# Kernel tuning notes

Measured on AMD Instinct MI355X. Metric: run time of the kernel, lower is better.

## Reference

```python
import jax, jax.numpy as jnp
import numpy as np

B, N, E, F, D = 8, 2000, 64000, 1024, 128
NEG_SLOPE = 0.01  # torch LeakyReLU default

def leaky(x):
    return jnp.where(x >= 0, x, NEG_SLOPE * x)

def gcn_conv(x, ei, W, b):
    # PyG GCNConv: add self loops, symmetric norm, x @ W, scatter-sum, + bias
    src, tgt = ei[0], ei[1]
    loops = jnp.arange(N, dtype=src.dtype)
    src_a = jnp.concatenate([src, loops])
    tgt_a = jnp.concatenate([tgt, loops])
    deg = jax.ops.segment_sum(jnp.ones(src_a.shape, x.dtype), tgt_a, num_segments=N)
    dinv = jnp.where(deg > 0, jax.lax.rsqrt(deg), 0.0)
    norm = dinv[src_a] * dinv[tgt_a]  # [E+N]
    h = x @ W                          # [N, F]
    out = jax.ops.segment_sum(norm[:, None] * h[src_a], tgt_a, num_segments=N)
    return out + b

gcn_conv_b = jax.vmap(gcn_conv, in_axes=(0, 0, None, None))

def setup_inputs() -> dict:
    key = jax.random.key(0)
    ks = jax.random.split(key, 16)
    s = lambda fan: 1.0 / np.sqrt(fan)
    return {
        "x1": jax.random.normal(ks[0], (B, N, F), jnp.float32),
        "ei1": jax.random.randint(ks[1], (B, 2, E), 0, N, jnp.int32),
        "x2": jax.random.normal(ks[2], (B, N, F), jnp.float32),
        "ei2": jax.random.randint(ks[3], (B, 2, E), 0, N, jnp.int32),
        "Wg1": jax.random.normal(ks[4], (F, F), jnp.float32) * s(F),
        "bg1": jnp.zeros((F,), jnp.float32),
        "Wf1": jax.random.normal(ks[5], (F, D), jnp.float32) * s(F),
        "bf1": jnp.zeros((D,), jnp.float32),
        "Wg2": jax.random.normal(ks[6], (F, F), jnp.float32) * s(F),
        "bg2": jnp.zeros((F,), jnp.float32),
        "Wf2": jax.random.normal(ks[7], (F, D), jnp.float32) * s(F),
        "bf2": jnp.zeros((D,), jnp.float32),
        "W1": jax.random.normal(ks[8], (2 * D, 256), jnp.float32) * s(2 * D),
        "b1": jnp.zeros((256,), jnp.float32),
        "W2": jax.random.normal(ks[9], (256, 64), jnp.float32) * s(256),
        "b2": jnp.zeros((64,), jnp.float32),
        "Wo": jax.random.normal(ks[10], (64, 1), jnp.float32) * s(64),
        "bo": jnp.zeros((1,), jnp.float32),
    }

def reference(x1, ei1, x2, ei2, Wg1, bg1, Wf1, bf1, Wg2, bg2, Wf2, bf2,
              W1, b1, W2, b2, Wo, bo):
    # branch 1
    h1 = leaky(gcn_conv_b(x1, ei1, Wg1, bg1))       # [B, N, F]
    g1 = jnp.mean(h1, axis=1)                        # [B, F]
    g1 = leaky(g1 @ Wf1 + bf1)                       # [B, D] (dropout = eval identity)
    # branch 2
    h2 = leaky(gcn_conv_b(x2, ei2, Wg2, bg2))
    g2 = jnp.mean(h2, axis=1)
    g2 = leaky(g2 @ Wf2 + bf2)
    # head
    xc = jnp.concatenate([g1, g2], axis=1)           # [B, 2D]
    xc = leaky(xc @ W1 + b1)
    xc = leaky(xc @ W2 + b2)
    return jax.nn.sigmoid(xc @ Wo + bo)              # [B, 1]
```

## Files before the change

### kernel.cpp

```cpp
#include <hip/hip_runtime.h>
#include <stdint.h>

#define B 8
#define NN 2000
#define EG 64000
#define FF 1024
#define DD 128
#define BK 32
#define NCHUNK 125
#define CG 5

#define NB_CONV 32000
#define NB_WT   2048
#define NB_DEG  4000
#define NTK 16
#define NB_G8 504

typedef short short8 __attribute__((ext_vector_type(8)));
typedef float f32x4 __attribute__((ext_vector_type(4)));
typedef float f32x2 __attribute__((ext_vector_type(2)));

__device__ __forceinline__ unsigned short f2bf(float f) {
    union { float f; unsigned int u; } v; v.f = f;
    unsigned int u = v.u;
    unsigned int r = u + 0x7FFFu + ((u >> 16) & 1u);
    return (unsigned short)(r >> 16);
}
__device__ __forceinline__ float leaky(float v) { return v >= 0.0f ? v : 0.01f * v; }

__device__ __forceinline__ void acc8p(f32x2* __restrict__ r, float w, uint4 v) {
    union { unsigned int u; float f; } c;
    f32x2 wv = {w, w};
    f32x2 h;
    c.u = v.x << 16;          h.x = c.f;
    c.u = v.x & 0xffff0000u;  h.y = c.f;
    r[0] += wv * h;
    c.u = v.y << 16;          h.x = c.f;
    c.u = v.y & 0xffff0000u;  h.y = c.f;
    r[1] += wv * h;
    c.u = v.z << 16;          h.x = c.f;
    c.u = v.z & 0xffff0000u;  h.y = c.f;
    r[2] += wv * h;
    c.u = v.w << 16;          h.x = c.f;
    c.u = v.w & 0xffff0000u;  h.y = c.f;
    r[3] += wv * h;
}

__global__ void k_prep(const float* __restrict__ x_a, const float* __restrict__ x_b,
                       unsigned short* __restrict__ xb,
                       const float* __restrict__ Wg_a, const float* __restrict__ Wg_b,
                       unsigned short* __restrict__ wT,
                       const int* __restrict__ ei_a, const int* __restrict__ ei_b,
                       int* __restrict__ degi) {
    int blk = blockIdx.x;
    int tid = threadIdx.x;
    __shared__ float tile[32][33];
    if (blk < NB_CONV) {
        int i = blk * 256 + tid;
        float4 v = (i < NB_CONV * 128) ? ((const float4*)x_a)[i]
                                       : ((const float4*)x_b)[i - NB_CONV * 128];
        ushort4 o;
        o.x = f2bf(v.x); o.y = f2bf(v.y); o.z = f2bf(v.z); o.w = f2bf(v.w);
        ((ushort4*)xb)[i] = o;
    } else if (blk < NB_CONV + NB_WT) {
        int b2 = blk - NB_CONV;
        int z = b2 >> 10, rem = b2 & 1023;
        int by = rem >> 5, bx = rem & 31;
        int tx = tid & 31, ty = tid >> 5;
        int k0 = by * 32, n0 = bx * 32;
        const float* Wg = z ? Wg_b : Wg_a;
        unsigned short* o = wT + (size_t)z * FF * FF;
#pragma unroll
        for (int r = 0; r < 4; ++r) {
            int row = ty + r * 8;
            tile[row][tx] = Wg[(k0 + row) * FF + n0 + tx];
        }
        __syncthreads();
#pragma unroll
        for (int r = 0; r < 4; ++r) {
            int row = ty + r * 8;
            o[(n0 + row) * FF + k0 + tx] = f2bf(tile[tx][row]);
        }
    } else {
        int i = (blk - NB_CONV - NB_WT) * 256 + tid;
        int g = i / EG, e = i - g * EG;
        const int* ei = (g < B) ? (ei_a + (size_t)g * 2 * EG)
                                : (ei_b + (size_t)(g - B) * 2 * EG);
        int t = ei[EG + e];
        atomicAdd(&degi[g * NN + t], 1);
    }
}

__global__ void k_scan(const int* __restrict__ degi, int* __restrict__ csr_off,
                       int* __restrict__ cursor, float* __restrict__ dinv) {
    int g = blockIdx.x, t = threadIdx.x;
    __shared__ int part[256];
    int loc[8];
    int s = 0;
#pragma unroll
    for (int i = 0; i < 8; ++i) {
        int n = t * 8 + i;
        int c = (n < NN) ? degi[g * NN + n] : 0;
        if (n < NN) dinv[g * NN + n] = rsqrtf((float)(c + 1));
        loc[i] = s;
        s += c;
    }
    part[t] = s;
    __syncthreads();
    for (int off = 1; off < 256; off <<= 1) {
        int v = (t >= off) ? part[t - off] : 0;
        __syncthreads();
        part[t] += v;
        __syncthreads();
    }
    int base = part[t] - s;
#pragma unroll
    for (int i = 0; i < 8; ++i) {
        int n = t * 8 + i;
        if (n < NN) {
            int o = base + loc[i];
            csr_off[g * (NN + 1) + n] = o;
            cursor[g * NN + n] = o;
        }
    }
    if (t == 255) csr_off[g * (NN + 1) + NN] = part[255];
}

__launch_bounds__(512, 2) __global__
void k_gemm8(const unsigned short* __restrict__ Abf, const unsigned short* __restrict__ wT,
             unsigned short* __restrict__ Hbf,
             const int* __restrict__ ei_a, const int* __restrict__ ei_b,
             int* __restrict__ cursor, const float* __restrict__ dinv,
             int2* __restrict__ epk) {
    __shared__ __align__(16) char smem[131072];
    int bid = blockIdx.x;
    int wg = (bid & 7) * 63 + (bid >> 3);
    int mt = wg >> 2, nt = wg & 3;
    int set = (mt >= 63) ? 1 : 0;
    int m0 = set * 16000 + (mt - set * 63) * 256;
    int n0 = nt * 256;
    int mlim = set * 16000 + 16000;
    const unsigned short* Bg = wT + (size_t)set * FF * FF;

    int tid = threadIdx.x;
    int lane = tid & 63, wave = tid >> 6;
    int wr = wave >> 2, wc = wave & 3;
    int l15 = lane & 15, q = lane >> 4;
    int qx = q ^ (((l15 >> 2) & 1) << 1);
    int arow = wr * 128 + l15;
    int brow = wc * 64 + l15;
    int col8s = (tid & 7) ^ (((tid >> 5) & 1) << 1);
    int srow = tid >> 3;
    unsigned wbase = (unsigned)wave << 10;

    f32x4 acc[8][4];
#pragma unroll
    for (int i = 0; i < 8; ++i)
#pragma unroll
        for (int j = 0; j < 4; ++j) acc[i][j] = (f32x4){0.f, 0.f, 0.f, 0.f};

    auto stage = [&](int ktn, int isB, int hh) {
        const unsigned short* gsrc = isB ? Bg : Abf;
        int x0 = isB ? n0 : m0;
        int r1 = x0 + hh * 128 + srow;
        int kb = ktn * 64 + col8s * 8;
        unsigned db = ((unsigned)(ktn & 1) << 16) | ((unsigned)isB << 15)
                    | ((unsigned)hh << 14) | wbase;
        __builtin_amdgcn_global_load_lds(
            (const __attribute__((address_space(1))) unsigned int*)(gsrc + (size_t)r1 * FF + kb),
            (__attribute__((address_space(3))) unsigned int*)&smem[db], 16, 0, 0);
        __builtin_amdgcn_global_load_lds(
            (const __attribute__((address_space(1))) unsigned int*)(gsrc + (size_t)(r1 + 64) * FF + kb),
            (__attribute__((address_space(3))) unsigned int*)&smem[db + 8192], 16, 0, 0);
    };

    stage(0, 0, 0); stage(0, 0, 1); stage(0, 1, 0); stage(0, 1, 1);

    unsigned bb = 0;
    auto lda = [&](int i, int kk) -> short8 {
        return *(const short8*)&smem[bb + ((unsigned)(arow + i * 16) << 7)
                                        + ((unsigned)(kk * 4 + qx) << 4)];
    };
    auto ldb = [&](int j, int kk) -> short8 {
        return *(const short8*)&smem[bb + 32768u + ((unsigned)(brow + j * 16) << 7)
                                        + ((unsigned)(kk * 4 + qx) << 4)];
    };

    for (int kt = 0; kt < NTK; ++kt) {
        asm volatile("s_waitcnt vmcnt(0)" ::: "memory");
        __builtin_amdgcn_s_barrier();
        bb = (unsigned)(kt & 1) << 16;
        short8 fa[4], fb[4];
#pragma unroll
        for (int j = 0; j < 4; ++j) fb[j] = ldb(j, 0);
#pragma unroll
        for (int i = 0; i < 4; ++i) fa[i] = lda(i, 0);
        if (kt + 1 < NTK) stage(kt + 1, 0, 0);
        __builtin_amdgcn_s_barrier();
        asm volatile("s_waitcnt lgkmcnt(0)" ::: "memory");
        __builtin_amdgcn_sched_barrier(0);
        __builtin_amdgcn_s_setprio(1);
#pragma unroll
        for (int i = 0; i < 4; ++i)
#pragma unroll
            for (int j = 0; j < 4; ++j)
                acc[i][j] = __builtin_amdgcn_mfma_f32_16x16x32_bf16(fa[i], fb[j], acc[i][j], 0, 0, 0);
        __builtin_amdgcn_s_setprio(0);
        __builtin_amdgcn_s_barrier();
#pragma unroll
        for (int i = 0; i < 4; ++i) fa[i] = lda(i + 4, 0);
        if (kt + 1 < NTK) stage(kt + 1, 0, 1);
        __builtin_amdgcn_s_barrier();
        asm volatile("s_waitcnt lgkmcnt(0)" ::: "memory");
        __builtin_amdgcn_sched_barrier(0);
        __builtin_amdgcn_s_setprio(1);
#pragma unroll
        for (int i = 0; i < 4; ++i)
#pragma unroll
            for (int j = 0; j < 4; ++j)
                acc[i + 4][j] = __builtin_amdgcn_mfma_f32_16x16x32_bf16(fa[i], fb[j], acc[i + 4][j], 0, 0, 0);
        __builtin_amdgcn_s_setprio(0);
        __builtin_amdgcn_s_barrier();
#pragma unroll
        for (int j = 0; j < 4; ++j) fb[j] = ldb(j, 1);
#pragma unroll
        for (int i = 0; i < 4; ++i) fa[i] = lda(i, 1);
        if (kt + 1 < NTK) stage(kt + 1, 1, 0);
        __builtin_amdgcn_s_barrier();
        asm volatile("s_waitcnt lgkmcnt(0)" ::: "memory");
        __builtin_amdgcn_sched_barrier(0);
        __builtin_amdgcn_s_setprio(1);
#pragma unroll
        for (int i = 0; i < 4; ++i)
#pragma unroll
            for (int j = 0; j < 4; ++j)
                acc[i][j] = __builtin_amdgcn_mfma_f32_16x16x32_bf16(fa[i], fb[j], acc[i][j], 0, 0, 0);
        __builtin_amdgcn_s_setprio(0);
        __builtin_amdgcn_s_barrier();
#pragma unroll
        for (int i = 0; i < 4; ++i) fa[i] = lda(i + 4, 1);
        if (kt + 1 < NTK) stage(kt + 1, 1, 1);
        __builtin_amdgcn_s_barrier();
        asm volatile("s_waitcnt lgkmcnt(0)" ::: "memory");
        __builtin_amdgcn_sched_barrier(0);
        __builtin_amdgcn_s_setprio(1);
#pragma unroll
        for (int i = 0; i < 4; ++i)
#pragma unroll
            for (int j = 0; j < 4; ++j)
                acc[i + 4][j] = __builtin_amdgcn_mfma_f32_16x16x32_bf16(fa[i], fb[j], acc[i + 4][j], 0, 0, 0);
        __builtin_amdgcn_s_setprio(0);
        __builtin_amdgcn_s_barrier();
    }

#pragma unroll
    for (int i = 0; i < 8; ++i) {
#pragma unroll
        for (int j = 0; j < 4; ++j) {
            int n = n0 + wc * 64 + j * 16 + l15;
#pragma unroll
            for (int v = 0; v < 4; ++v) {
                int m = m0 + wr * 128 + i * 16 + q * 4 + v;
                if (m < mlim) Hbf[(size_t)m * FF + n] = f2bf(acc[i][j][v]);
            }
        }
    }

    int ebase = bid * 512 + tid;
#pragma unroll
    for (int r = 0; r < 4; ++r) {
        int idx = ebase + r * (NB_G8 * 512);
        if (idx < 16 * EG) {
            int gg = idx / EG, e = idx - gg * EG;
            const int* ei = (gg < B) ? (ei_a + (size_t)gg * 2 * EG)
                                     : (ei_b + (size_t)(gg - B) * 2 * EG);
            int s = ei[e];
            int t = ei[EG + e];
            int pos = atomicAdd(&cursor[gg * NN + t], 1);
            int2 p;
            p.x = s;
            p.y = __float_as_int(dinv[gg * NN + s] * dinv[gg * NN + t]);
            epk[(size_t)gg * EG + pos] = p;
        }
    }
}

__launch_bounds__(256) __global__
void k_aggreduce(const unsigned short* __restrict__ Hbf, const int* __restrict__ csr_off,
                 const int2* __restrict__ epk, const float* __restrict__ dinv,
                 const float* __restrict__ bg_a, const float* __restrict__ bg_b,
                 float* __restrict__ part) {
    int blk = blockIdx.x;
    int phase = blk / 1000;
    int bp = blk - phase * 1000;
    int half = phase & 1;
    int g = (phase >> 1) * 8 + (bp & 7);
    int chunk = bp >> 3;
    int tid = threadIdx.x;
    int team = tid >> 6;
    int lane = tid & 63;
    int f0 = half * 512 + lane * 8;
    int n0 = chunk * 16 + team * 4;
    const unsigned short* Hb = Hbf + (size_t)g * NN * FF;
    const int2* ep = epk + (size_t)g * EG;
    const float* bg = (g < B) ? bg_a : bg_b;

    f32x2 bgv[4];
#pragma unroll
    for (int i = 0; i < 4; ++i) bgv[i] = (f32x2){bg[f0 + 2 * i], bg[f0 + 2 * i + 1]};
    f32x2 bsum[4];
#pragma unroll
    for (int i = 0; i < 4; ++i) bsum[i] = (f32x2){0.f, 0.f};

    for (int nn = 0; nn < 4; ++nn) {
        int n = n0 + nn;
        float dn = dinv[g * NN + n];
        int beg = csr_off[g * (NN + 1) + n];
        int end = csr_off[g * (NN + 1) + n + 1];
        f32x2 racc[4];
#pragma unroll
        for (int i = 0; i < 4; ++i) racc[i] = (f32x2){0.f, 0.f};
        {
            uint4 sv = *(const uint4*)&Hb[(n << 10) + f0];
            acc8p(racc, dn * dn, sv);
        }
        int j = beg;
        int2 pe0, pe1, pe2, pe3;
        if (j + 4 <= end) { pe0 = ep[j]; pe1 = ep[j + 1]; pe2 = ep[j + 2]; pe3 = ep[j + 3]; }
        for (; j + 8 <= end; j += 4) {
            int2 e0 = pe0, e1 = pe1, e2 = pe2, e3 = pe3;
            pe0 = ep[j + 4]; pe1 = ep[j + 5]; pe2 = ep[j + 6]; pe3 = ep[j + 7];
            uint4 v0 = *(const uint4*)&Hb[(e0.x << 10) + f0];
            uint4 v1 = *(const uint4*)&Hb[(e1.x << 10) + f0];
            uint4 v2 = *(const uint4*)&Hb[(e2.x << 10) + f0];
            uint4 v3 = *(const uint4*)&Hb[(e3.x << 10) + f0];
            acc8p(racc, __int_as_float(e0.y), v0);
            acc8p(racc, __int_as_float(e1.y), v1);
            acc8p(racc, __int_as_float(e2.y), v2);
            acc8p(racc, __int_as_float(e3.y), v3);
        }
        if (j + 4 <= end) {
            uint4 v0 = *(const uint4*)&Hb[(pe0.x << 10) + f0];
            uint4 v1 = *(const uint4*)&Hb[(pe1.x << 10) + f0];
            uint4 v2 = *(const uint4*)&Hb[(pe2.x << 10) + f0];
            uint4 v3 = *(const uint4*)&Hb[(pe3.x << 10) + f0];
            acc8p(racc, __int_as_float(pe0.y), v0);
            acc8p(racc, __int_as_float(pe1.y), v1);
            acc8p(racc, __int_as_float(pe2.y), v2);
            acc8p(racc, __int_as_float(pe3.y), v3);
            j += 4;
        }
        for (; j < end; ++j) {
            int2 e = ep[j];
            uint4 v = *(const uint4*)&Hb[(e.x << 10) + f0];
            acc8p(racc, __int_as_float(e.y), v);
        }
#pragma unroll
        for (int i = 0; i < 4; ++i) {
            f32x2 t = racc[i] + bgv[i];
            bsum[i].x += leaky(t.x);
            bsum[i].y += leaky(t.y);
        }
    }

    __shared__ float red[3][64 * 9];
    if (team > 0) {
#pragma unroll
        for (int i = 0; i < 4; ++i) {
            red[team - 1][lane * 9 + 2 * i]     = bsum[i].x;
            red[team - 1][lane * 9 + 2 * i + 1] = bsum[i].y;
        }
    }
    __syncthreads();
    if (team == 0) {
        float* o = part + ((size_t)g * NCHUNK + chunk) * FF + f0;
        float r[8];
#pragma unroll
        for (int i = 0; i < 4; ++i) {
            r[2 * i]     = bsum[i].x;
            r[2 * i + 1] = bsum[i].y;
        }
#pragma unroll
        for (int t = 0; t < 3; ++t)
#pragma unroll
            for (int i = 0; i < 8; ++i) r[i] += red[t][lane * 9 + i];
        float4 a = {r[0], r[1], r[2], r[3]};
        float4 c = {r[4], r[5], r[6], r[7]};
        *(float4*)&o[0] = a;
        *(float4*)&o[4] = c;
    }
}

__global__ void k_gsum1(const float* __restrict__ part, float* __restrict__ part2) {
    int blk = blockIdx.x;
    int g = blk / 20;
    int rem = blk - g * 20;
    int fq = rem / CG, cg = rem - fq * CG;
    int f = fq * 256 + threadIdx.x;
    const float* p = part + (size_t)g * NCHUNK * FF + (size_t)cg * 25 * FF + f;
    float s = 0.f;
#pragma unroll 5
    for (int c = 0; c < 25; ++c) s += p[(size_t)c * FF];
    part2[((size_t)g * CG + cg) * FF + f] = s;
}

__launch_bounds__(512) __global__
void k_fc(const float* __restrict__ part2, const float* __restrict__ Wf_a,
          const float* __restrict__ bf_a, const float* __restrict__ Wf_b,
          const float* __restrict__ bf_b, float* __restrict__ g12) {
    int g = blockIdx.x, t = threadIdx.x;
    int d = t & 127, slice = t >> 7;
    __shared__ float gs[FF];
    __shared__ float red[4][DD];
    const float* p = part2 + (size_t)g * CG * FF;
#pragma unroll
    for (int i = 0; i < 2; ++i) {
        int f = i * 512 + t;
        float s = 0.f;
#pragma unroll
        for (int c = 0; c < CG; ++c) s += p[(size_t)c * FF + f];
        gs[f] = s;
    }
    __syncthreads();
    const float* Wf = (g < B) ? Wf_a : Wf_b;
    const float* bfv = (g < B) ? bf_a : bf_b;
    float acc = 0.f;
    int fbase = slice * 256;
#pragma unroll 8
    for (int ff = 0; ff < 256; ++ff) {
        int f = fbase + ff;
        acc += gs[f] * Wf[f * DD + d];
    }
    red[slice][d] = acc;
    __syncthreads();
    if (t < DD) {
        float a = red[0][t] + red[1][t] + red[2][t] + red[3][t];
        a = a * (1.0f / (float)NN) + bfv[t];
        g12[g * DD + t] = leaky(a);
    }
}

__launch_bounds__(256) __global__
void k_head(const float* __restrict__ g, const float* __restrict__ W1, const float* __restrict__ b1,
            const float* __restrict__ W2, const float* __restrict__ b2,
            const float* __restrict__ Wo, const float* __restrict__ bo, float* __restrict__ out) {
    __shared__ float xc[8][256];
    __shared__ float l1[8][256];
    __shared__ float l2[8][64];
    int t = threadIdx.x;
#pragma unroll
    for (int i = 0; i < 8; ++i) {
        int idx = i * 256 + t;
        int b = idx >> 8, j = idx & 255;
        xc[b][j] = (j < DD) ? g[b * DD + j] : g[B * DD + b * DD + (j - DD)];
    }
    __syncthreads();
    {
        int j = t;
        float a[8];
#pragma unroll
        for (int b = 0; b < 8; ++b) a[b] = b1[j];
        for (int k = 0; k < 256; ++k) {
            float w = W1[k * 256 + j];
#pragma unroll
            for (int b = 0; b < 8; ++b) a[b] += xc[b][k] * w;
        }
#pragma unroll
        for (int b = 0; b < 8; ++b) l1[b][j] = leaky(a[b]);
    }
    __syncthreads();
    if (t < 64) {
        int j = t;
        float a[8];
#pragma unroll
        for (int b = 0; b < 8; ++b) a[b] = b2[j];
        for (int k = 0; k < 256; ++k) {
            float w = W2[k * 64 + j];
#pragma unroll
            for (int b = 0; b < 8; ++b) a[b] += l1[b][k] * w;
        }
#pragma unroll
        for (int b = 0; b < 8; ++b) l2[b][j] = leaky(a[b]);
    }
    __syncthreads();
    if (t < 8) {
        float a = bo[0];
        for (int k = 0; k < 64; ++k) a += l2[t][k] * Wo[k];
        out[t] = 1.0f / (1.0f + expf(-a));
    }
}

extern "C" void kernel_launch(void* const* d_in, const int* in_sizes, int n_in,
                              void* d_out, int out_size, void* d_ws, size_t ws_size,
                              hipStream_t stream) {
    const float* x1  = (const float*)d_in[0];
    const int*   ei1 = (const int*)d_in[1];
    const float* x2  = (const float*)d_in[2];
    const int*   ei2 = (const int*)d_in[3];
    const float* Wg1 = (const float*)d_in[4];
    const float* bg1 = (const float*)d_in[5];
    const float* Wf1 = (const float*)d_in[6];
    const float* bf1 = (const float*)d_in[7];
    const float* Wg2 = (const float*)d_in[8];
    const float* bg2 = (const float*)d_in[9];
    const float* Wf2 = (const float*)d_in[10];
    const float* bf2 = (const float*)d_in[11];
    const float* W1  = (const float*)d_in[12];
    const float* b1  = (const float*)d_in[13];
    const float* W2  = (const float*)d_in[14];
    const float* b2  = (const float*)d_in[15];
    const float* Wo  = (const float*)d_in[16];
    const float* bo  = (const float*)d_in[17];
    float* out = (float*)d_out;

    auto align = [](size_t v) { return (v + 255) & ~(size_t)255; };
    size_t need = 0;
    size_t o_deg  = need; need += align((size_t)16 * NN * 4);
    size_t o_dinv = need; need += align((size_t)16 * NN * 4);
    size_t o_csr  = need; need += align((size_t)16 * (NN + 1) * 4);
    size_t o_cur  = need; need += align((size_t)16 * NN * 4);
    size_t o_epk  = need; need += align((size_t)16 * EG * 8);
    size_t o_xbf  = need; need += align(((size_t)16 * NN + 128) * FF * 2);
    size_t o_wT   = need; need += align((size_t)2 * FF * FF * 2);
    size_t o_hbf  = need; need += align((size_t)16 * NN * FF * 2);
    size_t o_part = need; need += align((size_t)16 * NCHUNK * FF * 4);
    size_t o_pt2  = need; need += align((size_t)16 * CG * FF * 4);
    size_t o_g12  = need; need += align((size_t)16 * DD * 4);
    (void)need;

    char* w = (char*)d_ws;
    int* degi    = (int*)(w + o_deg);
    float* dinv  = (float*)(w + o_dinv);
    int* csr     = (int*)(w + o_csr);
    int* cur     = (int*)(w + o_cur);
    int2* epk    = (int2*)(w + o_epk);
    unsigned short* xbf = (unsigned short*)(w + o_xbf);
    unsigned short* wT  = (unsigned short*)(w + o_wT);
    unsigned short* hbf = (unsigned short*)(w + o_hbf);
    float* part  = (float*)(w + o_part);
    float* part2 = (float*)(w + o_pt2);
    float* g12   = (float*)(w + o_g12);

    hipMemsetAsync(degi, 0, (size_t)16 * NN * 4, stream);
    k_prep<<<NB_CONV + NB_WT + NB_DEG, 256, 0, stream>>>(x1, x2, xbf, Wg1, Wg2, wT,
                                                         ei1, ei2, degi);
    k_scan<<<16, 256, 0, stream>>>(degi, csr, cur, dinv);
    k_gemm8<<<NB_G8, 512, 0, stream>>>(xbf, wT, hbf, ei1, ei2, cur, dinv, epk);
    k_aggreduce<<<4000, 256, 0, stream>>>(hbf, csr, epk, dinv, bg1, bg2, part);
    k_gsum1<<<16 * 20, 256, 0, stream>>>(part, part2);
    k_fc<<<16, 512, 0, stream>>>(part2, Wf1, bf1, Wf2, bf2, g12);
    k_head<<<1, 256, 0, stream>>>(g12, W1, b1, W2, b2, Wo, bo, out);
}
```

Before: 544.0 us.

## Rework GEMM LDS swizzle, stage ordering and partial vmcnt waits

Changes the LDS XOR swizzle to an 8-way row-based pattern and precomputes the swizzled column offsets for each k-half. The staging order now loads B before A, and rows are split so each stage covers interleaved 64-row halves. The full vmcnt(0) wait at the top of each k-iteration is replaced by partial vmcnt(2) waits placed mid-iteration, so compute can begin once only part of the tile has landed. This is meant to reduce LDS bank conflicts and shorten stalls on global-to-LDS loads, but it makes the wait accounting fragile.

```diff
diff --git a/kernel.cpp b/kernel.cpp
--- a/kernel.cpp
+++ b/kernel.cpp
@@ -6,7 +6,6 @@
 #define EG 64000
 #define FF 1024
 #define DD 128
-#define BK 32
 #define NCHUNK 125
 #define CG 5
 
@@ -146,11 +145,13 @@
     int lane = tid & 63, wave = tid >> 6;
     int wr = wave >> 2, wc = wave & 3;
     int l15 = lane & 15, q = lane >> 4;
-    int qx = q ^ (((l15 >> 2) & 1) << 1);
     int arow = wr * 128 + l15;
     int brow = wc * 64 + l15;
-    int col8s = (tid & 7) ^ (((tid >> 5) & 1) << 1);
+    int sw = l15 & 7;
+    unsigned so0 = (unsigned)((q ^ sw) << 4);
+    unsigned so1 = (unsigned)(((4 + q) ^ sw) << 4);
     int srow = tid >> 3;
+    int col8s = (tid & 7) ^ (srow & 7);
     unsigned wbase = (unsigned)wave << 10;
 
     f32x4 acc[8][4];
@@ -159,43 +160,44 @@
 #pragma unroll
         for (int j = 0; j < 4; ++j) acc[i][j] = (f32x4){0.f, 0.f, 0.f, 0.f};
 
-    auto stage = [&](int ktn, int isB, int hh) {
+    auto stage = [&](int ktn, int isB, int h) {
         const unsigned short* gsrc = isB ? Bg : Abf;
         int x0 = isB ? n0 : m0;
-        int r1 = x0 + hh * 128 + srow;
+        int r1 = x0 + h * 64 + srow;
         int kb = ktn * 64 + col8s * 8;
         unsigned db = ((unsigned)(ktn & 1) << 16) | ((unsigned)isB << 15)
-                    | ((unsigned)hh << 14) | wbase;
+                    | ((unsigned)h << 13) | wbase | ((unsigned)(tid & 7) << 4)
+                    ;
+        db = ((unsigned)(ktn & 1) << 16) | ((unsigned)isB << 15)
+           | ((unsigned)h << 13) | wbase;
         __builtin_amdgcn_global_load_lds(
             (const __attribute__((address_space(1))) unsigned int*)(gsrc + (size_t)r1 * FF + kb),
             (__attribute__((address_space(3))) unsigned int*)&smem[db], 16, 0, 0);
         __builtin_amdgcn_global_load_lds(
-            (const __attribute__((address_space(1))) unsigned int*)(gsrc + (size_t)(r1 + 64) * FF + kb),
-            (__attribute__((address_space(3))) unsigned int*)&smem[db + 8192], 16, 0, 0);
+            (const __attribute__((address_space(1))) unsigned int*)(gsrc + (size_t)(r1 + 128) * FF + kb),
+            (__attribute__((address_space(3))) unsigned int*)&smem[db + 16384], 16, 0, 0);
     };
 
-    stage(0, 0, 0); stage(0, 0, 1); stage(0, 1, 0); stage(0, 1, 1);
+    stage(0, 1, 0); stage(0, 1, 1); stage(0, 0, 0); stage(0, 0, 1);
+    asm volatile("s_waitcnt vmcnt(2)" ::: "memory");
+    __builtin_amdgcn_s_barrier();
 
     unsigned bb = 0;
-    auto lda = [&](int i, int kk) -> short8 {
-        return *(const short8*)&smem[bb + ((unsigned)(arow + i * 16) << 7)
-                                        + ((unsigned)(kk * 4 + qx) << 4)];
+    auto lda = [&](int i, unsigned so) -> short8 {
+        return *(const short8*)&smem[bb + ((unsigned)(arow + i * 16) << 7) + so];
     };
-    auto ldb = [&](int j, int kk) -> short8 {
-        return *(const short8*)&smem[bb + 32768u + ((unsigned)(brow + j * 16) << 7)
-                                        + ((unsigned)(kk * 4 + qx) << 4)];
+    auto ldb = [&](int j, unsigned so) -> short8 {
+        return *(const short8*)&smem[bb + 32768u + ((unsigned)(brow + j * 16) << 7) + so];
     };
 
     for (int kt = 0; kt < NTK; ++kt) {
-        asm volatile("s_waitcnt vmcnt(0)" ::: "memory");
-        __builtin_amdgcn_s_barrier();
         bb = (unsigned)(kt & 1) << 16;
         short8 fa[4], fb[4];
 #pragma unroll
-        for (int j = 0; j < 4; ++j) fb[j] = ldb(j, 0);
-#pragma unroll
-        for (int i = 0; i < 4; ++i) fa[i] = lda(i, 0);
-        if (kt + 1 < NTK) stage(kt + 1, 0, 0);
+        for (int j = 0; j < 4; ++j) fb[j] = ldb(j, so0);
+#pragma unroll
+        for (int i = 0; i < 4; ++i) fa[i] = lda(i, so0);
+        if (kt + 1 < NTK) stage(kt + 1, 1, 0);
         __builtin_amdgcn_s_barrier();
         asm volatile("s_waitcnt lgkmcnt(0)" ::: "memory");
         __builtin_amdgcn_sched_barrier(0);
@@ -206,10 +208,12 @@
             for (int j = 0; j < 4; ++j)
                 acc[i][j] = __builtin_amdgcn_mfma_f32_16x16x32_bf16(fa[i], fb[j], acc[i][j], 0, 0, 0);
         __builtin_amdgcn_s_setprio(0);
-        __builtin_amdgcn_s_barrier();
-#pragma unroll
-        for (int i = 0; i < 4; ++i) fa[i] = lda(i + 4, 0);
-        if (kt + 1 < NTK) stage(kt + 1, 0, 1);
+        if (kt + 1 < NTK) asm volatile("s_waitcnt vmcnt(2)" ::: "memory");
+        else              asm volatile("s_waitcnt vmcnt(0)" ::: "memory");
+        __builtin_amdgcn_s_barrier();
+#pragma unroll
+        for (int i = 0; i < 4; ++i) fa[i] = lda(i + 4, so0);
+        if (kt + 1 < NTK) stage(kt + 1, 1, 1);
         __builtin_amdgcn_s_barrier();
         asm volatile("s_waitcnt lgkmcnt(0)" ::: "memory");
         __builtin_amdgcn_sched_barrier(0);
@@ -222,10 +226,10 @@
         __builtin_amdgcn_s_setprio(0);
         __builtin_amdgcn_s_barrier();
 #pragma unroll
-        for (int j = 0; j < 4; ++j) fb[j] = ldb(j, 1);
-#pragma unroll
-        for (int i = 0; i < 4; ++i) fa[i] = lda(i, 1);
-        if (kt + 1 < NTK) stage(kt + 1, 1, 0);
+        for (int j = 0; j < 4; ++j) fb[j] = ldb(j, so1);
+#pragma unroll
+        for (int i = 0; i < 4; ++i) fa[i] = lda(i, so1);
+        if (kt + 1 < NTK) stage(kt + 1, 0, 0);
         __builtin_amdgcn_s_barrier();
         asm volatile("s_waitcnt lgkmcnt(0)" ::: "memory");
         __builtin_amdgcn_sched_barrier(0);
@@ -238,8 +242,8 @@
         __builtin_amdgcn_s_setprio(0);
         __builtin_amdgcn_s_barrier();
 #pragma unroll
-        for (int i = 0; i < 4; ++i) fa[i] = lda(i + 4, 1);
-        if (kt + 1 < NTK) stage(kt + 1, 1, 1);
+        for (int i = 0; i < 4; ++i) fa[i] = lda(i + 4, so1);
+        if (kt + 1 < NTK) stage(kt + 1, 0, 1);
         __builtin_amdgcn_s_barrier();
         asm volatile("s_waitcnt lgkmcnt(0)" ::: "memory");
         __builtin_amdgcn_sched_barrier(0);
@@ -250,6 +254,7 @@
             for (int j = 0; j < 4; ++j)
                 acc[i + 4][j] = __builtin_amdgcn_mfma_f32_16x16x32_bf16(fa[i], fb[j], acc[i + 4][j], 0, 0, 0);
         __builtin_amdgcn_s_setprio(0);
+        asm volatile("s_waitcnt vmcnt(2)" ::: "memory");
         __builtin_amdgcn_s_barrier();
     }
 
```

After: 538.0 us. Within noise of the previous version (-1.1%).
